# Performance work log

Measured on AMD Instinct MI355X. Metric: run time of the kernel, lower is better.

## Reference

```python
import jax, jax.numpy as jnp
import numpy as np

B, N, DIM, HID, MAXN = 2048, 65536, 256, 512, 64
MID_KEY = (MAXN + HID) // 2   # 288
MID_VAL = (DIM + HID) // 2    # 384
MID_DEC = (HID + DIM) // 2    # 384
MID_SZ  = (HID + 1) // 2      # 256

def _ln(x, g, b):
    m = x.mean(-1, keepdims=True)
    v = ((x - m) ** 2).mean(-1, keepdims=True)
    return (x - m) * jax.lax.rsqrt(v + 1e-5) * g + b

def _mish(x):
    return x * jnp.tanh(jax.nn.softplus(x))

def _mlp_ln(x, W1, b1, g, be, W2, b2):
    return _mish(_ln(x @ W1 + b1, g, be)) @ W2 + b2

def _mlp(x, W1, b1, W2, b2):
    return _mish(x @ W1 + b1) @ W2 + b2

def setup_inputs():
    key = jax.random.key(0)
    ks = iter(jax.random.split(key, 40))
    def rn(shape, s=0.05):
        return jax.random.normal(next(ks), shape, jnp.float32) * s
    x = jax.random.normal(next(ks), (N, DIM), jnp.float32)
    batch = jnp.sort(jax.random.randint(next(ks), (N,), 0, B)).astype(jnp.int32)
    z32 = lambda *s: jnp.zeros(s, jnp.float32)
    o32 = lambda *s: jnp.ones(s, jnp.float32)
    return dict(
        x=x, batch=batch, n_batches=B,
        e_rank_W=rn((DIM, 1)), e_rank_b=z32(1),
        e_card_W=rn((1, HID)), e_card_b=z32(HID),
        e_key_W1=rn((MAXN, MID_KEY)), e_key_b1=z32(MID_KEY), e_key_g=o32(MID_KEY), e_key_be=z32(MID_KEY),
        e_key_W2=rn((MID_KEY, HID)), e_key_b2=z32(HID),
        e_val_W1=rn((DIM, MID_VAL)), e_val_b1=z32(MID_VAL), e_val_g=o32(MID_VAL), e_val_be=z32(MID_VAL),
        e_val_W2=rn((MID_VAL, HID)), e_val_b2=z32(HID),
        d_key_W1=rn((MAXN, MID_KEY)), d_key_b1=z32(MID_KEY), d_key_g=o32(MID_KEY), d_key_be=z32(MID_KEY),
        d_key_W2=rn((MID_KEY, HID)), d_key_b2=z32(HID),
        d_dec_W1=rn((HID, MID_DEC)), d_dec_b1=z32(MID_DEC),
        d_dec_W2=rn((MID_DEC, DIM)), d_dec_b2=z32(DIM),
        d_size_W1=rn((HID, MID_SZ)), d_size_b1=z32(MID_SZ), d_size_g=o32(MID_SZ), d_size_be=z32(MID_SZ),
        d_size_W2=rn((MID_SZ, 1)), d_size_b2=z32(1),
    )

def reference(x, batch, n_batches, e_rank_W, e_rank_b, e_card_W, e_card_b,
              e_key_W1, e_key_b1, e_key_g, e_key_be, e_key_W2, e_key_b2,
              e_val_W1, e_val_b1, e_val_g, e_val_be, e_val_W2, e_val_b2,
              d_key_W1, d_key_b1, d_key_g, d_key_be, d_key_W2, d_key_b2,
              d_dec_W1, d_dec_b1, d_dec_W2, d_dec_b2,
              d_size_W1, d_size_b1, d_size_g, d_size_be, d_size_W2, d_size_b2):
    max_n = e_key_W1.shape[0]
    n_pts = x.shape[0]
    # ---- Encoder ----
    n = jax.ops.segment_sum(jnp.ones(n_pts, jnp.float32), batch, num_segments=n_batches).astype(jnp.int32)
    mag = jnp.abs(x @ e_rank_W + e_rank_b)[:, 0]                 # [N]
    sort_key = batch.astype(jnp.float32) * jnp.max(mag) + mag    # sort within each set by |rank|
    idx = jnp.argsort(sort_key)
    xs = x[idx]
    starts = jnp.cumsum(n) - n                                   # per-set offsets (batch is sorted)
    pos_idx = jnp.arange(n_pts) - starts[batch]                  # rank within each set
    pos = jax.nn.one_hot(pos_idx, max_n, dtype=x.dtype)
    y = _mlp_ln(xs, e_val_W1, e_val_b1, e_val_g, e_val_be, e_val_W2, e_val_b2) \
      * _mlp_ln(pos, e_key_W1, e_key_b1, e_key_g, e_key_be, e_key_W2, e_key_b2)
    z = jax.ops.segment_sum(y, batch, num_segments=n_batches) \
      + n.astype(jnp.float32)[:, None] @ e_card_W + e_card_b     # [B, HID]
    # ---- Decoder ----
    n_logits = _mlp_ln(z, d_size_W1, d_size_b1, d_size_g, d_size_be, d_size_W2, d_size_b2)  # [B, 1]
    n_dec = jnp.clip(jnp.round(n_logits[:, 0]), 0, max_n).astype(jnp.int32)
    keys = _mlp_ln(jnp.eye(max_n, dtype=x.dtype),                # onehot positions 0..max_n-1
                   d_key_W1, d_key_b1, d_key_g, d_key_be, d_key_W2, d_key_b2)  # [max_n, HID]
    zp = z[:, None, :] * keys[None, :, :]                        # [B, max_n, HID] (repeat_interleave -> dense+mask)
    xf = _mlp(zp, d_dec_W1, d_dec_b1, d_dec_W2, d_dec_b2)        # [B, max_n, DIM]
    mask = jnp.arange(max_n)[None, :] < n_dec[:, None]           # valid rows per set
    x_out = (xf * mask[..., None].astype(xf.dtype)).reshape(-1, xf.shape[-1])
    batch_out = jnp.repeat(jnp.arange(n_batches, dtype=jnp.int32), max_n)
    return x_out, batch_out, mask.reshape(-1)
```

## Files before the change

### kernel.cpp

```cpp
#include <hip/hip_runtime.h>

#define NPTS   65536
#define NB     2048
#define DIMX   256
#define HIDN   512
#define MAXNN  64
#define MIDK   288
#define MIDV   384
#define MIDD   384
#define MIDS   256

typedef unsigned short ushort_t;
typedef __attribute__((ext_vector_type(8))) short short8;
typedef __attribute__((ext_vector_type(4))) float f32x4;

__device__ __forceinline__ float mishf(float x) {
    float e = __expf(fminf(x, 30.f));
    float n = e * (e + 2.f);
    return x * n * __builtin_amdgcn_rcpf(n + 2.f);
}
__device__ __forceinline__ ushort_t f2bf(float f) {
    unsigned u = __float_as_uint(f);
    u += 0x7fffu + ((u >> 16) & 1u);
    return (ushort_t)(u >> 16);
}
__device__ __forceinline__ float bf2f(ushort_t h) {
    return __uint_as_float(((unsigned)h) << 16);
}
__device__ __forceinline__ void dma16(const void* g, void* lds) {
    __builtin_amdgcn_global_load_lds(
        (const __attribute__((address_space(1))) unsigned int*)g,
        (__attribute__((address_space(3))) unsigned int*)lds, 16, 0, 0);
}
__device__ __forceinline__ int lbound(const int* __restrict__ a, int lo, int hi, int v) {
    while (lo < hi) { int m = (lo + hi) >> 1; if (a[m] < v) lo = m + 1; else hi = m; }
    return lo;
}

__global__ __launch_bounds__(256)
void k_mag(const float* __restrict__ x, const float* __restrict__ rW,
           const float* __restrict__ rb, float* __restrict__ mag,
           unsigned int* __restrict__ maxmag, ushort_t* __restrict__ xb)
{
    const int lane = threadIdx.x & 63;
    const int wave = threadIdx.x >> 6;
    const int gw = blockIdx.x * 4 + wave;
    float4 wv = *(const float4*)(rW + lane * 4);
    float bias = rb[0];
    float lmax = 0.f;
    for (int pt = gw; pt < NPTS; pt += 16384) {
        float4 xv = *(const float4*)(x + (size_t)pt * DIMX + lane * 4);
        ushort4 u;
        u.x = f2bf(xv.x); u.y = f2bf(xv.y); u.z = f2bf(xv.z); u.w = f2bf(xv.w);
        *(ushort4*)(xb + (size_t)pt * DIMX + lane * 4) = u;
        double d = (double)xv.x * wv.x + (double)xv.y * wv.y
                 + (double)xv.z * wv.z + (double)xv.w * wv.w;
        #pragma unroll
        for (int o = 32; o > 0; o >>= 1) d += __shfl_xor(d, o);
        float s = fabsf((float)(d + (double)bias));
        if (lane == 0) mag[pt] = s;
        lmax = fmaxf(lmax, s);
    }
    __shared__ float wm[4];
    if (lane == 0) wm[wave] = lmax;
    __syncthreads();
    if (threadIdx.x == 0) {
        float m = fmaxf(fmaxf(wm[0], wm[1]), fmaxf(wm[2], wm[3]));
        atomicMax(maxmag, __float_as_uint(m));
    }
}

__global__ __launch_bounds__(256)
void k_rank(const int* __restrict__ batch, const float* __restrict__ mag,
            const unsigned int* __restrict__ maxmag, int* __restrict__ kidx)
{
    int i = blockIdx.x * 256 + threadIdx.x;
    if (i >= NPTS) return;
    int b = batch[i];
    int s = lbound(batch, 0, NPTS, b);
    int e = lbound(batch, s, NPTS, b + 1);
    float M = __uint_as_float(*maxmag);
    float kb = __fmul_rn((float)b, M);
    float ki = __fadd_rn(kb, mag[i]);
    int r = 0;
    for (int j = s; j < e; ++j) {
        float kj = __fadd_rn(kb, mag[j]);
        r += (kj < ki) || (kj == ki && j < i);
    }
    kidx[i] = (r < MAXNN) ? r : MAXNN;
}

__global__ __launch_bounds__(512)
void k_setup(const float* __restrict__ eW1, const float* __restrict__ eb1,
             const float* __restrict__ eg, const float* __restrict__ ebe,
             const float* __restrict__ eW2, const float* __restrict__ eb2,
             const float* __restrict__ dW1, const float* __restrict__ db1,
             const float* __restrict__ dg, const float* __restrict__ dbe,
             const float* __restrict__ dW2, const float* __restrict__ db2,
             float* __restrict__ enc_tbl, float* __restrict__ dec_tbl,
             const int* __restrict__ batch, const float* __restrict__ cardW,
             const float* __restrict__ cardb, float* __restrict__ z,
             const float* __restrict__ V0, ushort_t* __restrict__ T0,
             const float* __restrict__ V1, ushort_t* __restrict__ T1,
             const float* __restrict__ V2, ushort_t* __restrict__ T2,
             const float* __restrict__ V3, ushort_t* __restrict__ T3,
             unsigned int* __restrict__ maxmag)
{
    const int blk = blockIdx.x;
    const int t = threadIdx.x;
    if (blk == 0 && t == 0) *maxmag = 0u;
    if (blk < 129) {
        const float *W1, *b1, *g, *be, *W2, *b2; float* out; int wrow;
        if (blk < 65) {
            W1 = eW1; b1 = eb1; g = eg; be = ebe; W2 = eW2; b2 = eb2;
            out = enc_tbl + blk * HIDN; wrow = (blk < 64) ? blk : -1;
        } else {
            int r = blk - 65;
            W1 = dW1; b1 = db1; g = dg; be = dbe; W2 = dW2; b2 = db2;
            out = dec_tbl + r * HIDN; wrow = r;
        }
        __shared__ float h[MIDK];
        __shared__ float red[512];
        float v = 0.f;
        if (t < MIDK) v = b1[t] + (wrow >= 0 ? W1[wrow * MIDK + t] : 0.f);
        red[t] = (t < MIDK) ? v : 0.f;
        __syncthreads();
        for (int o = 256; o > 0; o >>= 1) { if (t < o) red[t] += red[t + o]; __syncthreads(); }
        float m = red[0] / (float)MIDK;
        __syncthreads();
        float d = v - m;
        red[t] = (t < MIDK) ? d * d : 0.f;
        __syncthreads();
        for (int o = 256; o > 0; o >>= 1) { if (t < o) red[t] += red[t + o]; __syncthreads(); }
        float rs = rsqrtf(red[0] / (float)MIDK + 1e-5f);
        __syncthreads();
        if (t < MIDK) h[t] = mishf(d * rs * g[t] + be[t]);
        __syncthreads();
        float acc = b2[t];
        #pragma unroll 8
        for (int k = 0; k < MIDK; ++k) acc = fmaf(h[k], W2[k * HIDN + t], acc);
        out[t] = acc;
    } else if (blk < 129 + NB) {
        int b = blk - 129;
        int s = lbound(batch, 0, NPTS, b);
        int e = lbound(batch, s, NPTS, b + 1);
        float n = (float)(e - s);
        z[b * HIDN + t] = fmaf(n, cardW[t], cardb[t]);
    } else {
        int idx = (blk - (129 + NB)) * 512 + t;
        const float* W; ushort_t* T; int N, K, off;
        if (idx < 98304)       { W = V0; T = T0; K = 256; N = 384; off = idx; }
        else if (idx < 294912) { W = V1; T = T1; K = 384; N = 512; off = idx - 98304; }
        else if (idx < 491520) { W = V2; T = T2; K = 512; N = 384; off = idx - 294912; }
        else                   { W = V3; T = T3; K = 384; N = 256; off = idx - 491520; }
        int k = off / N, n = off - k * N;
        T[(size_t)n * K + k] = f2bf(W[off]);
    }
}

__global__ __launch_bounds__(256)
void k_size(const float* __restrict__ z, const float* __restrict__ W1,
            const float* __restrict__ b1, const float* __restrict__ g,
            const float* __restrict__ be, const float* __restrict__ W2,
            const float* __restrict__ b2, int* __restrict__ ndec)
{
    const int b0 = blockIdx.x * 4, t = threadIdx.x;
    __shared__ float zr[4][HIDN];
    __shared__ float red[4][256];
    #pragma unroll
    for (int gI = 0; gI < 4; ++gI) {
        zr[gI][t] = z[(b0 + gI) * HIDN + t];
        zr[gI][t + 256] = z[(b0 + gI) * HIDN + 256 + t];
    }
    __syncthreads();
    float acc[4];
    float bb1 = b1[t];
    #pragma unroll
    for (int gI = 0; gI < 4; ++gI) acc[gI] = bb1;
    #pragma unroll 8
    for (int k = 0; k < HIDN; ++k) {
        float wv = W1[k * MIDS + t];
        #pragma unroll
        for (int gI = 0; gI < 4; ++gI) acc[gI] = fmaf(zr[gI][k], wv, acc[gI]);
    }
    #pragma unroll
    for (int gI = 0; gI < 4; ++gI) red[gI][t] = acc[gI];
    __syncthreads();
    for (int o = 128; o > 0; o >>= 1) {
        if (t < o) {
            #pragma unroll
            for (int gI = 0; gI < 4; ++gI) red[gI][t] += red[gI][t + o];
        }
        __syncthreads();
    }
    float mm[4];
    #pragma unroll
    for (int gI = 0; gI < 4; ++gI) mm[gI] = red[gI][0] * (1.f / 256.f);
    __syncthreads();
    #pragma unroll
    for (int gI = 0; gI < 4; ++gI) { float d = acc[gI] - mm[gI]; red[gI][t] = d * d; }
    __syncthreads();
    for (int o = 128; o > 0; o >>= 1) {
        if (t < o) {
            #pragma unroll
            for (int gI = 0; gI < 4; ++gI) red[gI][t] += red[gI][t + o];
        }
        __syncthreads();
    }
    float rs[4];
    #pragma unroll
    for (int gI = 0; gI < 4; ++gI) rs[gI] = rsqrtf(red[gI][0] * (1.f / 256.f) + 1e-5f);
    __syncthreads();
    float w2 = W2[t], gg = g[t], bbe = be[t];
    #pragma unroll
    for (int gI = 0; gI < 4; ++gI) {
        float h = mishf((acc[gI] - mm[gI]) * rs[gI] * gg + bbe);
        red[gI][t] = h * w2;
    }
    __syncthreads();
    for (int o = 128; o > 0; o >>= 1) {
        if (t < o) {
            #pragma unroll
            for (int gI = 0; gI < 4; ++gI) red[gI][t] += red[gI][t + o];
        }
        __syncthreads();
    }
    if (t < 4) {
        float logit = red[t][0] + b2[0];
        float n = rintf(logit);
        n = fminf(fmaxf(n, 0.f), 64.f);
        ndec[b0 + t] = (int)n;
    }
}

__global__ __launch_bounds__(256)
void k_post(const int* __restrict__ ndec, float* __restrict__ out_x,
            float* __restrict__ outb, float* __restrict__ outm,
            int* __restrict__ rowmap, int* __restrict__ cntpad)
{
    const int gidx = blockIdx.x * 256 + threadIdx.x;
    float4 z4 = make_float4(0.f, 0.f, 0.f, 0.f);
    float4* p = (float4*)out_x;
    #pragma unroll
    for (int i = 0; i < 32; ++i) p[gidx + i * 262144] = z4;
    if (gidx < NB * MAXNN) {
        outb[gidx] = (float)(gidx >> 6);
        outm[gidx] = ((gidx & 63) < ndec[gidx >> 6]) ? 1.f : 0.f;
    }
    if (blockIdx.x == 0) {
        __shared__ int lcnt;
        if (threadIdx.x == 0) lcnt = 0;
        __syncthreads();
        for (int b = threadIdx.x; b < NB; b += 256) {
            int n = ndec[b];
            if (n > 0) {
                int base = atomicAdd(&lcnt, n);
                for (int q = 0; q < n; ++q) rowmap[base + q] = b * 64 + q;
            }
        }
        __syncthreads();
        int c = lcnt;
        int pad = (c + 127) & ~127;
        for (int i = c + threadIdx.x; i < pad; i += 256) rowmap[i] = -1;
        if (threadIdx.x == 0) *cntpad = pad;
    }
}

__global__ __launch_bounds__(512, 2)
void k_mm_e1f(const ushort_t* __restrict__ A, const ushort_t* __restrict__ Bt,
              const float* __restrict__ bias, const float* __restrict__ g,
              const float* __restrict__ be, ushort_t* __restrict__ C)
{
    const int m0 = blockIdx.x * 128;
    __shared__ __align__(16) ushort_t As[128 * 64];
    __shared__ __align__(16) ushort_t Bs[384 * 64];
    const int t = threadIdx.x;
    const int l = t & 63;
    const int w = t >> 6;
    const int wm = (w >> 2) * 64;
    const int wq = (w & 3) * 96;
    const int l4 = (l >> 4) << 2;
    const int drow = l >> 3;
    const int dblk = (l & 7) ^ drow;

    f32x4 acc[4][6];
    #pragma unroll
    for (int a = 0; a < 4; ++a)
        #pragma unroll
        for (int b = 0; b < 6; ++b) acc[a][b] = (f32x4)0.f;

    for (int k0 = 0; k0 < DIMX; k0 += 64) {
        #pragma unroll
        for (int ii = 0; ii < 2; ++ii) {
            int i = w * 2 + ii;
            dma16(A + (size_t)(m0 + i * 8 + drow) * DIMX + k0 + dblk * 8, &As[i * 512]);
        }
        #pragma unroll
        for (int ii = 0; ii < 6; ++ii) {
            int i = w * 6 + ii;
            dma16(Bt + (size_t)(i * 8 + drow) * DIMX + k0 + dblk * 8, &Bs[i * 512]);
        }
        __syncthreads();
        #pragma unroll
        for (int ks = 0; ks < 2; ++ks) {
            int kq = ks * 4 + (l >> 4);
            short8 af[4], bfr[6];
            #pragma unroll
            for (int fm = 0; fm < 4; ++fm) {
                int row = wm + fm * 16 + (l & 15);
                af[fm] = *(const short8*)&As[row * 64 + ((kq ^ (row & 7)) << 3)];
            }
            #pragma unroll
            for (int fn = 0; fn < 6; ++fn) {
                int row = wq + fn * 16 + (l & 15);
                bfr[fn] = *(const short8*)&Bs[row * 64 + ((kq ^ (row & 7)) << 3)];
            }
            #pragma unroll
            for (int fm = 0; fm < 4; ++fm)
                #pragma unroll
                for (int fn = 0; fn < 6; ++fn)
                    acc[fm][fn] = __builtin_amdgcn_mfma_f32_16x16x32_bf16(
                        af[fm], bfr[fn], acc[fm][fn], 0, 0, 0);
        }
        __syncthreads();
    }

    float bb[6], gg[6], bee[6];
    #pragma unroll
    for (int fn = 0; fn < 6; ++fn) {
        int col = wq + fn * 16 + (l & 15);
        bb[fn] = bias[col]; gg[fn] = g[col]; bee[fn] = be[col];
    }
    #pragma unroll
    for (int fm = 0; fm < 4; ++fm)
        #pragma unroll
        for (int fn = 0; fn < 6; ++fn)
            #pragma unroll
            for (int j = 0; j < 4; ++j) acc[fm][fn][j] += bb[fn];

    float* ssum = (float*)As;
    float* ssq  = ssum + 512;
    #pragma unroll
    for (int fm = 0; fm < 4; ++fm) {
        #pragma unroll
        for (int j = 0; j < 4; ++j) {
            float s = 0.f, q = 0.f;
            #pragma unroll
            for (int fn = 0; fn < 6; ++fn) {
                float v = acc[fm][fn][j];
                s += v; q += v * v;
            }
            #pragma unroll
            for (int o = 1; o < 16; o <<= 1) {
                s += __shfl_xor(s, o);
                q += __shfl_xor(q, o);
            }
            if ((l & 15) == 0) {
                int r = wm + fm * 16 + l4 + j;
                ssum[r * 4 + (w & 3)] = s;
                ssq[r * 4 + (w & 3)] = q;
            }
        }
    }
    __syncthreads();
    #pragma unroll
    for (int fm = 0; fm < 4; ++fm) {
        #pragma unroll
        for (int j = 0; j < 4; ++j) {
            int r = wm + fm * 16 + l4 + j;
            float s = ssum[r * 4 + 0] + ssum[r * 4 + 1] + ssum[r * 4 + 2] + ssum[r * 4 + 3];
            float q = ssq[r * 4 + 0] + ssq[r * 4 + 1] + ssq[r * 4 + 2] + ssq[r * 4 + 3];
            float m = s * (1.f / 384.f);
            float var = q * (1.f / 384.f) - m * m;
            float rs = rsqrtf(var + 1e-5f);
            #pragma unroll
            for (int fn = 0; fn < 6; ++fn) {
                float v = (acc[fm][fn][j] - m) * rs * gg[fn] + bee[fn];
                C[(size_t)(m0 + r) * MIDV + wq + fn * 16 + (l & 15)] = f2bf(mishf(v));
            }
        }
    }
}

__global__ __launch_bounds__(256, 2)
void k_mm_e2(const ushort_t* __restrict__ A, const ushort_t* __restrict__ Bt,
             const float* __restrict__ bias, int K, const float* __restrict__ tbl,
             const int* __restrict__ kidx, const int* __restrict__ batch,
             float* __restrict__ zout)
{
    const int flat = blockIdx.y * gridDim.x + blockIdx.x;
    const int nx = gridDim.x;
    const int xcd = flat & 7;
    const int lin = flat >> 3;
    const int n0 = (lin % nx) * 128;
    const int m0 = ((lin / nx) + ((gridDim.y >> 3) * xcd)) * 128;
    __shared__ __align__(16) ushort_t sAB[2 * 128 * 64];
    __shared__ int barr[128];
    __shared__ int karr[128];
    ushort_t* As = sAB;
    ushort_t* Bs = sAB + 128 * 64;
    const int t = threadIdx.x;
    const int l = t & 63;
    const int w = t >> 6;
    const int wm = (w >> 1) * 64;
    const int wn = (w & 1) * 64;
    const int l4 = (l >> 4) << 2;
    const int drow = l >> 3;
    const int dblk = (l & 7) ^ drow;

    if (t < 128) { barr[t] = batch[m0 + t]; karr[t] = kidx[m0 + t]; }

    f32x4 acc[4][4];
    #pragma unroll
    for (int a = 0; a < 4; ++a)
        #pragma unroll
        for (int b = 0; b < 4; ++b) acc[a][b] = (f32x4)0.f;

    for (int k0 = 0; k0 < K; k0 += 64) {
        #pragma unroll
        for (int ii = 0; ii < 4; ++ii) {
            int i = w * 4 + ii;
            dma16(A + (size_t)(m0 + i * 8 + drow) * K + k0 + dblk * 8, &As[i * 512]);
        }
        #pragma unroll
        for (int ii = 0; ii < 4; ++ii) {
            int i = w * 4 + ii;
            dma16(Bt + (size_t)(n0 + i * 8 + drow) * K + k0 + dblk * 8, &Bs[i * 512]);
        }
        __syncthreads();
        #pragma unroll
        for (int ks = 0; ks < 2; ++ks) {
            short8 af[4], bfr[4];
            int kq = ks * 4 + (l >> 4);
            #pragma unroll
            for (int fm = 0; fm < 4; ++fm) {
                int row = wm + fm * 16 + (l & 15);
                af[fm] = *(const short8*)&As[row * 64 + ((kq ^ (row & 7)) << 3)];
            }
            #pragma unroll
            for (int fn = 0; fn < 4; ++fn) {
                int row = wn + fn * 16 + (l & 15);
                bfr[fn] = *(const short8*)&Bs[row * 64 + ((kq ^ (row & 7)) << 3)];
            }
            #pragma unroll
            for (int fm = 0; fm < 4; ++fm)
                #pragma unroll
                for (int fn = 0; fn < 4; ++fn)
                    acc[fm][fn] = __builtin_amdgcn_mfma_f32_16x16x32_bf16(
                        af[fm], bfr[fn], acc[fm][fn], 0, 0, 0);
        }
        __syncthreads();
    }

    float* yred = (float*)sAB;
    #pragma unroll
    for (int pass = 0; pass < 2; ++pass) {
        if ((w >> 1) == pass) {
            #pragma unroll
            for (int fn = 0; fn < 4; ++fn) {
                int cl = wn + fn * 16 + (l & 15);
                float bbv = bias[n0 + cl];
                #pragma unroll
                for (int fm = 0; fm < 4; ++fm) {
                    #pragma unroll
                    for (int j = 0; j < 4; ++j) {
                        int rl = fm * 16 + l4 + j;
                        float v = (acc[fm][fn][j] + bbv)
                                * tbl[karr[pass * 64 + rl] * HIDN + (n0 + cl)];
                        yred[cl * 64 + (rl ^ (cl & 31))] = v;
                    }
                }
            }
        }
        __syncthreads();
        {
            int c = t & 127, q = t >> 7;
            int gc = n0 + c;
            float run = 0.f; int curb = -1;
            #pragma unroll
            for (int ch = 0; ch < 2; ++ch) {
                float v16[16]; int b16[16];
                #pragma unroll
                for (int rr = 0; rr < 16; ++rr) {
                    int rl = q * 32 + ch * 16 + rr;
                    v16[rr] = yred[c * 64 + (rl ^ (c & 31))];
                    b16[rr] = barr[pass * 64 + rl];
                }
                #pragma unroll
                for (int rr = 0; rr < 16; ++rr) {
                    if (b16[rr] != curb) {
                        if (curb >= 0) atomicAdd(&zout[curb * HIDN + gc], run);
                        curb = b16[rr]; run = v16[rr];
                    } else run += v16[rr];
                }
            }
            atomicAdd(&zout[curb * HIDN + gc], run);
        }
        __syncthreads();
    }
}

template<int MODE>
__device__ __forceinline__
void mm_body(const ushort_t* __restrict__ A, const ushort_t* __restrict__ Bt,
             const float* __restrict__ bias, void* __restrict__ Cptr, int K,
             const float* __restrict__ tbl, const float* __restrict__ zin,
             const int* __restrict__ rowmap, const int* __restrict__ cntpad)
{
    const int flat = blockIdx.y * gridDim.x + blockIdx.x;
    const int nx = gridDim.x;
    const int xcd = flat & 7;
    const int lin = flat >> 3;
    const int n0 = (lin % nx) * 128;
    const int m0 = ((lin / nx) + ((gridDim.y >> 3) * xcd)) * 128;
    if (m0 >= *cntpad) return;
    __shared__ __align__(16) ushort_t sAB[2 * 128 * 64];
    ushort_t* As = sAB;
    ushort_t* Bs = sAB + 128 * 64;
    const int t = threadIdx.x;
    const int l = t & 63;
    const int w = t >> 6;
    const int wm = (w >> 1) * 64;
    const int wn = (w & 1) * 64;
    const int l4 = (l >> 4) << 2;
    const int drow = l >> 3;
    const int dblk = (l & 7) ^ drow;

    int g4[4], p4[4];
    if (MODE == 2) {
        #pragma unroll
        for (int ii = 0; ii < 4; ++ii) {
            int i = w * 4 + ii;
            int gr = rowmap[m0 + i * 8 + drow];
            if (gr < 0) gr = 0;
            g4[ii] = gr >> 6; p4[ii] = gr & 63;
        }
    }

    f32x4 acc[4][4];
    #pragma unroll
    for (int a = 0; a < 4; ++a)
        #pragma unroll
        for (int b = 0; b < 4; ++b) acc[a][b] = (f32x4)0.f;

    for (int k0 = 0; k0 < K; k0 += 64) {
        if (MODE == 2) {
            #pragma unroll
            for (int ii = 0; ii < 4; ++ii) {
                int i = w * 4 + ii;
                int row = i * 8 + drow;
                const float* zp = zin + g4[ii] * HIDN + k0 + dblk * 8;
                const float* kp = tbl + p4[ii] * HIDN + k0 + dblk * 8;
                float4 z0 = *(const float4*)zp;
                float4 z1 = *(const float4*)(zp + 4);
                float4 q0 = *(const float4*)kp;
                float4 q1 = *(const float4*)(kp + 4);
                ushort4 u0, u1;
                u0.x = f2bf(z0.x * q0.x); u0.y = f2bf(z0.y * q0.y);
                u0.z = f2bf(z0.z * q0.z); u0.w = f2bf(z0.w * q0.w);
                u1.x = f2bf(z1.x * q1.x); u1.y = f2bf(z1.y * q1.y);
                u1.z = f2bf(z1.z * q1.z); u1.w = f2bf(z1.w * q1.w);
                ushort_t* dst = &As[row * 64 + (l & 7) * 8];
                *(ushort4*)dst = u0;
                *(ushort4*)(dst + 4) = u1;
            }
        } else {
            #pragma unroll
            for (int ii = 0; ii < 4; ++ii) {
                int i = w * 4 + ii;
                const ushort_t* gp = A + (size_t)(m0 + i * 8 + drow) * K + k0 + dblk * 8;
                dma16(gp, &As[i * 512]);
            }
        }
        #pragma unroll
        for (int ii = 0; ii < 4; ++ii) {
            int i = w * 4 + ii;
            const ushort_t* gp = Bt + (size_t)(n0 + i * 8 + drow) * K + k0 + dblk * 8;
            dma16(gp, &Bs[i * 512]);
        }
        __syncthreads();
        #pragma unroll
        for (int ks = 0; ks < 2; ++ks) {
            short8 af[4], bfr[4];
            int kq = ks * 4 + (l >> 4);
            #pragma unroll
            for (int fm = 0; fm < 4; ++fm) {
                int row = wm + fm * 16 + (l & 15);
                af[fm] = *(const short8*)&As[row * 64 + ((kq ^ (row & 7)) << 3)];
            }
            #pragma unroll
            for (int fn = 0; fn < 4; ++fn) {
                int row = wn + fn * 16 + (l & 15);
                bfr[fn] = *(const short8*)&Bs[row * 64 + ((kq ^ (row & 7)) << 3)];
            }
            #pragma unroll
            for (int fm = 0; fm < 4; ++fm)
                #pragma unroll
                for (int fn = 0; fn < 4; ++fn)
                    acc[fm][fn] = __builtin_amdgcn_mfma_f32_16x16x32_bf16(
                        af[fm], bfr[fn], acc[fm][fn], 0, 0, 0);
        }
        __syncthreads();
    }

    if (MODE == 2) {
        ushort_t* C = (ushort_t*)Cptr;
        #pragma unroll
        for (int fm = 0; fm < 4; ++fm) {
            int gr0 = m0 + wm + fm * 16 + l4;
            #pragma unroll
            for (int fn = 0; fn < 4; ++fn) {
                int gc = n0 + wn + fn * 16 + (l & 15);
                float bbv = bias[gc];
                #pragma unroll
                for (int j = 0; j < 4; ++j)
                    C[(size_t)(gr0 + j) * MIDD + gc] = f2bf(mishf(acc[fm][fn][j] + bbv));
            }
        }
    } else {
        float* C = (float*)Cptr;
        #pragma unroll
        for (int fm = 0; fm < 4; ++fm) {
            int gr0 = m0 + wm + fm * 16 + l4;
            int om[4];
            #pragma unroll
            for (int j = 0; j < 4; ++j) om[j] = rowmap[gr0 + j];
            #pragma unroll
            for (int fn = 0; fn < 4; ++fn) {
                int gc = n0 + wn + fn * 16 + (l & 15);
                float bbv = bias[gc];
                #pragma unroll
                for (int j = 0; j < 4; ++j)
                    if (om[j] >= 0) C[(size_t)om[j] * DIMX + gc] = acc[fm][fn][j] + bbv;
            }
        }
    }
}

__global__ __launch_bounds__(256, 2)
void k_mm_d1(const ushort_t* Bt, const float* bias, void* C, int K,
             const float* tbl, const float* zin, const int* rowmap, const int* cntpad)
{ mm_body<2>(nullptr, Bt, bias, C, K, tbl, zin, rowmap, cntpad); }

__global__ __launch_bounds__(256, 2)
void k_mm_d2(const ushort_t* A, const ushort_t* Bt, const float* bias, void* C, int K,
             const int* rowmap, const int* cntpad)
{ mm_body<3>(A, Bt, bias, C, K, nullptr, nullptr, rowmap, cntpad); }

extern "C" void kernel_launch(void* const* d_in, const int* in_sizes, int n_in,
                              void* d_out, int out_size, void* d_ws, size_t ws_size,
                              hipStream_t stream)
{
    const float* x        = (const float*)d_in[0];
    const int*   batch    = (const int*)  d_in[1];
    const float* e_rank_W = (const float*)d_in[3];
    const float* e_rank_b = (const float*)d_in[4];
    const float* e_card_W = (const float*)d_in[5];
    const float* e_card_b = (const float*)d_in[6];
    const float* e_key_W1 = (const float*)d_in[7];
    const float* e_key_b1 = (const float*)d_in[8];
    const float* e_key_g  = (const float*)d_in[9];
    const float* e_key_be = (const float*)d_in[10];
    const float* e_key_W2 = (const float*)d_in[11];
    const float* e_key_b2 = (const float*)d_in[12];
    const float* e_val_W1 = (const float*)d_in[13];
    const float* e_val_b1 = (const float*)d_in[14];
    const float* e_val_g  = (const float*)d_in[15];
    const float* e_val_be = (const float*)d_in[16];
    const float* e_val_W2 = (const float*)d_in[17];
    const float* e_val_b2 = (const float*)d_in[18];
    const float* d_key_W1 = (const float*)d_in[19];
    const float* d_key_b1 = (const float*)d_in[20];
    const float* d_key_g  = (const float*)d_in[21];
    const float* d_key_be = (const float*)d_in[22];
    const float* d_key_W2 = (const float*)d_in[23];
    const float* d_key_b2 = (const float*)d_in[24];
    const float* d_dec_W1 = (const float*)d_in[25];
    const float* d_dec_b1 = (const float*)d_in[26];
    const float* d_dec_W2 = (const float*)d_in[27];
    const float* d_dec_b2 = (const float*)d_in[28];
    const float* d_size_W1= (const float*)d_in[29];
    const float* d_size_b1= (const float*)d_in[30];
    const float* d_size_g = (const float*)d_in[31];
    const float* d_size_be= (const float*)d_in[32];
    const float* d_size_W2= (const float*)d_in[33];
    const float* d_size_b2= (const float*)d_in[34];

    char* ws = (char*)d_ws;
    unsigned int* maxmag  = (unsigned int*)(ws + 8448);
    int*          kidx    = (int*)         (ws + 8704);
    float*        mag     = (float*)       (ws + 270848);
    float*        enc_tbl = (float*)       (ws + 532992);
    float*        dec_tbl = (float*)       (ws + 666112);
    float*        z       = (float*)       (ws + 797184);
    int*          ndec    = (int*)         (ws + 4991488);
    int*          cntpad  = (int*)         (ws + 4999684);
    int*          rowmap  = (int*)         (ws + 5000192);
    ushort_t*     evW1t   = (ushort_t*)    (ws + 5524480);
    ushort_t*     evW2t   = (ushort_t*)    (ws + 5721088);
    ushort_t*     ddW1t   = (ushort_t*)    (ws + 6114304);
    ushort_t*     ddW2t   = (ushort_t*)    (ws + 6507520);
    ushort_t*     xb      = (ushort_t*)    (ws + 6704384);
    ushort_t*     Hb      = (ushort_t*)    (ws + 6704384 + 33554432);
    ushort_t*     Hd      = (ushort_t*)    (ws + 6704384 + 33554432);

    float* out_x = (float*)d_out;
    float* out_b = out_x + (size_t)NB * MAXNN * DIMX;
    float* out_m = out_b + NB * MAXNN;

    k_setup<<<dim3(129 + NB + 1152), dim3(512), 0, stream>>>(
        e_key_W1, e_key_b1, e_key_g, e_key_be, e_key_W2, e_key_b2,
        d_key_W1, d_key_b1, d_key_g, d_key_be, d_key_W2, d_key_b2,
        enc_tbl, dec_tbl, batch, e_card_W, e_card_b, z,
        e_val_W1, evW1t, e_val_W2, evW2t, d_dec_W1, ddW1t, d_dec_W2, ddW2t,
        maxmag);
    k_mag<<<dim3(4096), dim3(256), 0, stream>>>(x, e_rank_W, e_rank_b, mag, maxmag, xb);
    k_rank<<<dim3(256), dim3(256), 0, stream>>>(batch, mag, maxmag, kidx);

    k_mm_e1f<<<dim3(512), dim3(512), 0, stream>>>(xb, evW1t, e_val_b1,
                                                  e_val_g, e_val_be, Hb);
    k_mm_e2<<<dim3(4, 512), dim3(256), 0, stream>>>(Hb, evW2t, e_val_b2, MIDV,
                                                    enc_tbl, kidx, batch, z);

    k_size<<<dim3(NB / 4), dim3(256), 0, stream>>>(z, d_size_W1, d_size_b1, d_size_g,
                                                   d_size_be, d_size_W2, d_size_b2, ndec);
    k_post<<<dim3(1024), dim3(256), 0, stream>>>(ndec, out_x, out_b, out_m,
                                                 rowmap, cntpad);
    k_mm_d1<<<dim3(3, 1024), dim3(256), 0, stream>>>(ddW1t, d_dec_b1, Hd, HIDN,
                                                     dec_tbl, z, rowmap, cntpad);
    k_mm_d2<<<dim3(2, 1024), dim3(256), 0, stream>>>(Hd, ddW2t, d_dec_b2, out_x, MIDD,
                                                     rowmap, cntpad);
}
```

Before: 484.6 us.

## Fuse magnitude pass into setup kernel and tile weight transposes through LDS

Folds the k_mag projection and bf16-conversion pass into the k_setup launch as extra blocks, which removes one kernel launch and the global atomic max. Each block now writes its own max to a blockmax array, and k_rank reduces those per block. The weight transpose is changed from one-element-per-thread strided writes to 64x64 LDS-tiled transposes so both reads and writes coalesce. The cost is that every k_rank block redundantly reduces 2048 partial maxima, and the workspace at offset 0 is reused for blockmax.

```diff
diff --git a/kernel.cpp b/kernel.cpp
--- a/kernel.cpp
+++ b/kernel.cpp
@@ -37,58 +37,10 @@
     return lo;
 }
 
-__global__ __launch_bounds__(256)
-void k_mag(const float* __restrict__ x, const float* __restrict__ rW,
-           const float* __restrict__ rb, float* __restrict__ mag,
-           unsigned int* __restrict__ maxmag, ushort_t* __restrict__ xb)
-{
-    const int lane = threadIdx.x & 63;
-    const int wave = threadIdx.x >> 6;
-    const int gw = blockIdx.x * 4 + wave;
-    float4 wv = *(const float4*)(rW + lane * 4);
-    float bias = rb[0];
-    float lmax = 0.f;
-    for (int pt = gw; pt < NPTS; pt += 16384) {
-        float4 xv = *(const float4*)(x + (size_t)pt * DIMX + lane * 4);
-        ushort4 u;
-        u.x = f2bf(xv.x); u.y = f2bf(xv.y); u.z = f2bf(xv.z); u.w = f2bf(xv.w);
-        *(ushort4*)(xb + (size_t)pt * DIMX + lane * 4) = u;
-        double d = (double)xv.x * wv.x + (double)xv.y * wv.y
-                 + (double)xv.z * wv.z + (double)xv.w * wv.w;
-        #pragma unroll
-        for (int o = 32; o > 0; o >>= 1) d += __shfl_xor(d, o);
-        float s = fabsf((float)(d + (double)bias));
-        if (lane == 0) mag[pt] = s;
-        lmax = fmaxf(lmax, s);
-    }
-    __shared__ float wm[4];
-    if (lane == 0) wm[wave] = lmax;
-    __syncthreads();
-    if (threadIdx.x == 0) {
-        float m = fmaxf(fmaxf(wm[0], wm[1]), fmaxf(wm[2], wm[3]));
-        atomicMax(maxmag, __float_as_uint(m));
-    }
-}
-
-__global__ __launch_bounds__(256)
-void k_rank(const int* __restrict__ batch, const float* __restrict__ mag,
-            const unsigned int* __restrict__ maxmag, int* __restrict__ kidx)
-{
-    int i = blockIdx.x * 256 + threadIdx.x;
-    if (i >= NPTS) return;
-    int b = batch[i];
-    int s = lbound(batch, 0, NPTS, b);
-    int e = lbound(batch, s, NPTS, b + 1);
-    float M = __uint_as_float(*maxmag);
-    float kb = __fmul_rn((float)b, M);
-    float ki = __fadd_rn(kb, mag[i]);
-    int r = 0;
-    for (int j = s; j < e; ++j) {
-        float kj = __fadd_rn(kb, mag[j]);
-        r += (kj < ki) || (kj == ki && j < i);
-    }
-    kidx[i] = (r < MAXNN) ? r : MAXNN;
-}
+#define SETUP_TBL   129
+#define SETUP_Z     (SETUP_TBL + NB)
+#define SETUP_WT    (SETUP_Z + 144)
+#define SETUP_TOTAL (SETUP_WT + 2048)
 
 __global__ __launch_bounds__(512)
 void k_setup(const float* __restrict__ eW1, const float* __restrict__ eb1,
@@ -104,12 +56,13 @@
              const float* __restrict__ V1, ushort_t* __restrict__ T1,
              const float* __restrict__ V2, ushort_t* __restrict__ T2,
              const float* __restrict__ V3, ushort_t* __restrict__ T3,
-             unsigned int* __restrict__ maxmag)
+             const float* __restrict__ x, const float* __restrict__ rW,
+             const float* __restrict__ rb, float* __restrict__ mag,
+             float* __restrict__ blockmax, ushort_t* __restrict__ xb)
 {
     const int blk = blockIdx.x;
     const int t = threadIdx.x;
-    if (blk == 0 && t == 0) *maxmag = 0u;
-    if (blk < 129) {
+    if (blk < SETUP_TBL) {
         const float *W1, *b1, *g, *be, *W2, *b2; float* out; int wrow;
         if (blk < 65) {
             W1 = eW1; b1 = eb1; g = eg; be = ebe; W2 = eW2; b2 = eb2;
@@ -140,22 +93,92 @@
         #pragma unroll 8
         for (int k = 0; k < MIDK; ++k) acc = fmaf(h[k], W2[k * HIDN + t], acc);
         out[t] = acc;
-    } else if (blk < 129 + NB) {
-        int b = blk - 129;
+    } else if (blk < SETUP_Z) {
+        int b = blk - SETUP_TBL;
         int s = lbound(batch, 0, NPTS, b);
         int e = lbound(batch, s, NPTS, b + 1);
         float n = (float)(e - s);
         z[b * HIDN + t] = fmaf(n, cardW[t], cardb[t]);
+    } else if (blk < SETUP_WT) {
+        int tile = blk - SETUP_Z;
+        const float* W; ushort_t* T; int K, N;
+        if (tile < 24)       { W = V0; T = T0; K = 256; N = 384; }
+        else if (tile < 72)  { tile -= 24;  W = V1; T = T1; K = 384; N = 512; }
+        else if (tile < 120) { tile -= 72;  W = V2; T = T2; K = 512; N = 384; }
+        else                 { tile -= 120; W = V3; T = T3; K = 384; N = 256; }
+        int ntn = N >> 6;
+        int k0 = (tile / ntn) * 64, n0 = (tile % ntn) * 64;
+        __shared__ float lds[64][65];
+        #pragma unroll
+        for (int pass = 0; pass < 8; ++pass) {
+            int kk = pass * 8 + (t >> 6);
+            lds[kk][t & 63] = W[(size_t)(k0 + kk) * N + n0 + (t & 63)];
+        }
+        __syncthreads();
+        #pragma unroll
+        for (int pass = 0; pass < 8; ++pass) {
+            int nn = pass * 8 + (t >> 6);
+            T[(size_t)(n0 + nn) * K + k0 + (t & 63)] = f2bf(lds[t & 63][nn]);
+        }
     } else {
-        int idx = (blk - (129 + NB)) * 512 + t;
-        const float* W; ushort_t* T; int N, K, off;
-        if (idx < 98304)       { W = V0; T = T0; K = 256; N = 384; off = idx; }
-        else if (idx < 294912) { W = V1; T = T1; K = 384; N = 512; off = idx - 98304; }
-        else if (idx < 491520) { W = V2; T = T2; K = 512; N = 384; off = idx - 294912; }
-        else                   { W = V3; T = T3; K = 384; N = 256; off = idx - 491520; }
-        int k = off / N, n = off - k * N;
-        T[(size_t)n * K + k] = f2bf(W[off]);
-    }
+        int mw = blk - SETUP_WT;
+        const int lane = t & 63;
+        const int w = t >> 6;
+        int gw = mw * 8 + w;
+        float4 wv = *(const float4*)(rW + lane * 4);
+        float bias = rb[0];
+        float lmax = 0.f;
+        for (int pt = gw; pt < NPTS; pt += 16384) {
+            float4 xv = *(const float4*)(x + (size_t)pt * DIMX + lane * 4);
+            ushort4 u;
+            u.x = f2bf(xv.x); u.y = f2bf(xv.y); u.z = f2bf(xv.z); u.w = f2bf(xv.w);
+            *(ushort4*)(xb + (size_t)pt * DIMX + lane * 4) = u;
+            double d = (double)xv.x * wv.x + (double)xv.y * wv.y
+                     + (double)xv.z * wv.z + (double)xv.w * wv.w;
+            #pragma unroll
+            for (int o = 32; o > 0; o >>= 1) d += __shfl_xor(d, o);
+            float s = fabsf((float)(d + (double)bias));
+            if (lane == 0) mag[pt] = s;
+            lmax = fmaxf(lmax, s);
+        }
+        __shared__ float wm8[8];
+        if (lane == 0) wm8[w] = lmax;
+        __syncthreads();
+        if (t == 0) {
+            float m = wm8[0];
+            #pragma unroll
+            for (int i = 1; i < 8; ++i) m = fmaxf(m, wm8[i]);
+            blockmax[mw] = m;
+        }
+    }
+}
+
+__global__ __launch_bounds__(256)
+void k_rank(const int* __restrict__ batch, const float* __restrict__ mag,
+            const float* __restrict__ blockmax, int* __restrict__ kidx)
+{
+    __shared__ float red[256];
+    const int t = threadIdx.x;
+    float m = 0.f;
+    for (int i = t; i < 2048; i += 256) m = fmaxf(m, blockmax[i]);
+    red[t] = m;
+    __syncthreads();
+    for (int o = 128; o > 0; o >>= 1) { if (t < o) red[t] = fmaxf(red[t], red[t + o]); __syncthreads(); }
+    float M = red[0];
+
+    int i = blockIdx.x * 256 + t;
+    if (i >= NPTS) return;
+    int b = batch[i];
+    int s = lbound(batch, 0, NPTS, b);
+    int e = lbound(batch, s, NPTS, b + 1);
+    float kb = __fmul_rn((float)b, M);
+    float ki = __fadd_rn(kb, mag[i]);
+    int r = 0;
+    for (int j = s; j < e; ++j) {
+        float kj = __fadd_rn(kb, mag[j]);
+        r += (kj < ki) || (kj == ki && j < i);
+    }
+    kidx[i] = (r < MAXNN) ? r : MAXNN;
 }
 
 __global__ __launch_bounds__(256)
@@ -687,7 +710,7 @@
     const float* d_size_b2= (const float*)d_in[34];
 
     char* ws = (char*)d_ws;
-    unsigned int* maxmag  = (unsigned int*)(ws + 8448);
+    float*        blockmax= (float*)       (ws + 0);
     int*          kidx    = (int*)         (ws + 8704);
     float*        mag     = (float*)       (ws + 270848);
     float*        enc_tbl = (float*)       (ws + 532992);
@@ -708,14 +731,13 @@
     float* out_b = out_x + (size_t)NB * MAXNN * DIMX;
     float* out_m = out_b + NB * MAXNN;
 
-    k_setup<<<dim3(129 + NB + 1152), dim3(512), 0, stream>>>(
+    k_setup<<<dim3(SETUP_TOTAL), dim3(512), 0, stream>>>(
         e_key_W1, e_key_b1, e_key_g, e_key_be, e_key_W2, e_key_b2,
         d_key_W1, d_key_b1, d_key_g, d_key_be, d_key_W2, d_key_b2,
         enc_tbl, dec_tbl, batch, e_card_W, e_card_b, z,
         e_val_W1, evW1t, e_val_W2, evW2t, d_dec_W1, ddW1t, d_dec_W2, ddW2t,
-        maxmag);
-    k_mag<<<dim3(4096), dim3(256), 0, stream>>>(x, e_rank_W, e_rank_b, mag, maxmag, xb);
-    k_rank<<<dim3(256), dim3(256), 0, stream>>>(batch, mag, maxmag, kidx);
+        x, e_rank_W, e_rank_b, mag, blockmax, xb);
+    k_rank<<<dim3(256), dim3(256), 0, stream>>>(batch, mag, blockmax, kidx);
 
     k_mm_e1f<<<dim3(512), dim3(512), 0, stream>>>(xb, evW1t, e_val_b1,
                                                   e_val_g, e_val_be, Hb);
```

New measurement: 449.7 us, median of 2. 7.2% less time.
